# Kernel optimization log

Hardware: AMD Instinct MI355X
Metric: run time of the kernel (lower is better)

Reference implementation:

```python
import jax, jax.numpy as jnp
import numpy as np

N_NODES = 100000
N_EDGES = 1600000
N_GRAPHS = 2048
HID = 64
IN_F = 14
N_CLS = 2
EPS = 1e-5


def _gcn_conv(x, row, col, w_edge, W, b, n_nodes):
    # PyG GCNConv with add_self_loops=True, normalize=True.
    xw = x @ W  # [N, out]
    # degree on target nodes, self-loop contributes weight 1
    deg = jnp.zeros((n_nodes,), x.dtype).at[col].add(w_edge) + 1.0
    dinv = deg ** -0.5
    norm = dinv[row] * w_edge * dinv[col]  # [E]
    out = jnp.zeros_like(xw).at[col].add(norm[:, None] * xw[row])
    out = out + (dinv * dinv)[:, None] * xw  # self-loop term
    return out + b


def _bn_relu(x, gamma, beta):
    mean = jnp.mean(x, axis=0)
    var = jnp.var(x, axis=0)  # biased, as PyTorch BN training normalization
    y = gamma * (x - mean) * jax.lax.rsqrt(var + EPS) + beta
    return jax.nn.relu(y)


def setup_inputs() -> dict:
    key = jax.random.key(0)
    ks = jax.random.split(key, 8)
    x = jax.random.normal(ks[0], (N_NODES, IN_F), dtype=jnp.float32)
    edge_index = jax.random.randint(ks[1], (2, N_EDGES), 0, N_NODES, dtype=jnp.int64)
    batch = jnp.sort(jax.random.randint(ks[2], (N_NODES,), 0, N_GRAPHS, dtype=jnp.int64))
    edge_weight = jnp.ones((N_EDGES,), dtype=jnp.float32)
    def lin(k, fi, fo):
        s = 1.0 / np.sqrt(fi)
        kw, kb = jax.random.split(k)
        return (jax.random.uniform(kw, (fi, fo), jnp.float32, -s, s),
                jax.random.uniform(kb, (fo,), jnp.float32, -s, s))
    W1, b1 = lin(ks[3], IN_F, HID)
    W2, b2 = lin(ks[4], HID, HID)
    W3, b3 = lin(ks[5], HID, HID)
    fcW, fcb = lin(ks[6], HID, N_CLS)
    g = jnp.ones((HID,), jnp.float32)
    z = jnp.zeros((HID,), jnp.float32)
    return {
        "x": x, "edge_index": edge_index, "batch": batch, "edge_weight": edge_weight,
        "W1": W1, "b1": b1, "W2": W2, "b2": b2, "W3": W3, "b3": b3,
        "g1": g, "bt1": z, "g2": g, "bt2": z, "g3": g, "bt3": z,
        "fcW": fcW, "fcb": fcb,
    }


def reference(x, edge_index, batch, edge_weight, W1, b1, W2, b2, W3, b3,
              g1, bt1, g2, bt2, g3, bt3, fcW, fcb):
    row, col = edge_index[0], edge_index[1]
    n = x.shape[0]
    h = _bn_relu(_gcn_conv(x, row, col, edge_weight, W1, b1, n), g1, bt1)
    h = _bn_relu(_gcn_conv(h, row, col, edge_weight, W2, b2, n), g2, bt2)
    h = _bn_relu(_gcn_conv(h, row, col, edge_weight, W3, b3, n), g3, bt3)
    node_embs = h  # dropout p=0 is identity
    graph_emb = jax.ops.segment_sum(node_embs, batch, num_segments=N_GRAPHS)
    out = graph_emb @ fcW + fcb
    return (out, node_embs, graph_emb)
```

## Files before the change

kernel.cpp:

```cpp
#include <hip/hip_runtime.h>

#define N_NODES 100000
#define N_EDGES 1600000
#define EMAX    2400000
#define N_GRAPHS 2048
#define HID 64
#define IN_F 14
#define N_CLS 2
#define EPS 1e-5f

#define BSHIFT 9
#define NBUCK 196
#define ABLOCKS 256
#define CHUNK (N_EDGES / ABLOCKS)

#define NBLK2 128
#define NCHUNK2 ((N_NODES + NBLK2 - 1) / NBLK2)

typedef _Float16 half_t;
typedef _Float16 half8 __attribute__((ext_vector_type(8)));
typedef float f32x4 __attribute__((ext_vector_type(4)));
typedef unsigned int uint4v __attribute__((ext_vector_type(4)));

#define GSTRIDE ((size_t)N_NODES * 16)


__global__ __launch_bounds__(256) void histA_kernel(const int* __restrict__ col,
                                                    int* __restrict__ histG) {
    __shared__ int hl[NBUCK];
    for (int i = threadIdx.x; i < NBUCK; i += 256) hl[i] = 0;
    __syncthreads();
    int e0 = blockIdx.x * CHUNK;
    for (int e = e0 + threadIdx.x; e < e0 + CHUNK; e += 256)
        atomicAdd(&hl[col[e] >> BSHIFT], 1);
    __syncthreads();
    for (int i = threadIdx.x; i < NBUCK; i += 256)
        histG[i * ABLOCKS + blockIdx.x] = hl[i];
}

__global__ __launch_bounds__(256) void scanS1_kernel(const int* __restrict__ histG,
                                                     int* __restrict__ bsumA) {
    __shared__ int ls[256];
    ls[threadIdx.x] = histG[blockIdx.x * 256 + threadIdx.x];
    __syncthreads();
    for (int off = 128; off > 0; off >>= 1) {
        if (threadIdx.x < off) ls[threadIdx.x] += ls[threadIdx.x + off];
        __syncthreads();
    }
    if (threadIdx.x == 0) bsumA[blockIdx.x] = ls[0];
}

__global__ __launch_bounds__(512) void topscan_kernel(int* __restrict__ bsum, int nb) {
    __shared__ int ls[512];
    int t = threadIdx.x;
    int v = (t < nb) ? bsum[t] : 0;
    ls[t] = v;
    __syncthreads();
    for (int off = 1; off < 512; off <<= 1) {
        int x = ls[t];
        if (t >= off) x += ls[t - off];
        __syncthreads();
        ls[t] = x;
        __syncthreads();
    }
    if (t < nb) bsum[t] = ls[t] - v;
}

__global__ __launch_bounds__(256) void scanS3_kernel(int* __restrict__ histG,
                                                     const int* __restrict__ bsumA,
                                                     int* __restrict__ ptr) {
    __shared__ int ls[256];
    int idx = blockIdx.x * 256 + threadIdx.x;
    int v = histG[idx];
    ls[threadIdx.x] = v;
    __syncthreads();
    for (int off = 1; off < 256; off <<= 1) {
        int x = ls[threadIdx.x];
        if (threadIdx.x >= off) x += ls[threadIdx.x - off];
        __syncthreads();
        ls[threadIdx.x] = x;
        __syncthreads();
    }
    histG[idx] = ls[threadIdx.x] - v + bsumA[blockIdx.x];
    if (blockIdx.x == 0 && threadIdx.x == 0) ptr[N_NODES] = N_EDGES;
}

__global__ __launch_bounds__(256) void scatterA_kernel(const int* __restrict__ row,
                                                       const int* __restrict__ col,
                                                       const float* __restrict__ w,
                                                       const int* __restrict__ histG,
                                                       int2* __restrict__ EA) {
    __shared__ int cur[NBUCK];
    for (int i = threadIdx.x; i < NBUCK; i += 256)
        cur[i] = histG[i * ABLOCKS + blockIdx.x];
    __syncthreads();
    int e0 = blockIdx.x * CHUNK;
    for (int e = e0 + threadIdx.x; e < e0 + CHUNK; e += 256) {
        int c = col[e];
        int r = row[e];
        int fx = (int)__float2uint_rn(w[e] * 8192.0f);
        int pos = atomicAdd(&cur[c >> BSHIFT], 1);
        EA[pos] = make_int2(r, (fx << 17) | c);
    }
}

__global__ __launch_bounds__(256) void bucket_kernel(const int2* __restrict__ EA,
                                                     const int* __restrict__ bsumA,
                                                     int2* __restrict__ EB,
                                                     int* __restrict__ ptr,
                                                     float* __restrict__ dinv) {
    __shared__ int hist[512], wsum[512], cur[512];
    int b = blockIdx.x;
    int beg = bsumA[b];
    int end = (b == NBUCK - 1) ? N_EDGES : bsumA[b + 1];
    int i0 = threadIdx.x, i1 = threadIdx.x + 256;
    hist[i0] = 0; hist[i1] = 0;
    wsum[i0] = 0; wsum[i1] = 0;
    __syncthreads();
    for (int e = beg + threadIdx.x; e < end; e += 256) {
        int2 ed = EA[e];
        int c9 = ed.y & 511;
        atomicAdd(&hist[c9], 1);
        atomicAdd(&wsum[c9], (int)((unsigned int)ed.y >> 17));
    }
    __syncthreads();
    int cnt0 = hist[i0], cnt1 = hist[i1];
    for (int off = 1; off < 512; off <<= 1) {
        int v0 = hist[i0], v1 = hist[i1];
        int a0 = (i0 >= off) ? hist[i0 - off] : 0;
        int a1 = (i1 >= off) ? hist[i1 - off] : 0;
        __syncthreads();
        hist[i0] = v0 + a0;
        hist[i1] = v1 + a1;
        __syncthreads();
    }
    int excl0 = hist[i0] - cnt0, excl1 = hist[i1] - cnt1;
    cur[i0] = beg + excl0;
    cur[i1] = beg + excl1;
    int col0 = (b << BSHIFT) + i0, col1 = (b << BSHIFT) + i1;
    if (col0 < N_NODES) {
        ptr[col0] = beg + excl0;
        dinv[col0] = rsqrtf(1.0f + (float)wsum[i0] * (1.0f / 8192.0f));
    }
    if (col1 < N_NODES) {
        ptr[col1] = beg + excl1;
        dinv[col1] = rsqrtf(1.0f + (float)wsum[i1] * (1.0f / 8192.0f));
    }
    __syncthreads();
    for (int e = beg + threadIdx.x; e < end; e += 256) {
        int2 ed = EA[e];
        int pos = atomicAdd(&cur[ed.y & 511], 1);
        EB[pos] = ed;
    }
}


__global__ __launch_bounds__(256) void histD_kernel(const int* __restrict__ ptr,
                                                    int* __restrict__ histD) {
    __shared__ int hl[2048];
    for (int i = threadIdx.x; i < 2048; i += 256) hl[i] = 0;
    __syncthreads();
    int n0 = blockIdx.x * NCHUNK2;
    int n1 = n0 + NCHUNK2; if (n1 > N_NODES) n1 = N_NODES;
    for (int n = n0 + threadIdx.x; n < n1; n += 256) {
        int d = ptr[n + 1] - ptr[n];
        if (d > 255) d = 255;
        atomicAdd(&hl[((threadIdx.x & 7) << 8) + d], 1);
    }
    __syncthreads();
    int s = 0;
#pragma unroll
    for (int c = 0; c < 8; c++) s += hl[(c << 8) + threadIdx.x];
    histD[threadIdx.x * NBLK2 + blockIdx.x] = s;
}

__global__ __launch_bounds__(128) void scanD1_kernel(const int* __restrict__ histD,
                                                     int* __restrict__ rowTot) {
    __shared__ int ls[128];
    ls[threadIdx.x] = histD[blockIdx.x * NBLK2 + threadIdx.x];
    __syncthreads();
    for (int off = 64; off > 0; off >>= 1) {
        if (threadIdx.x < off) ls[threadIdx.x] += ls[threadIdx.x + off];
        __syncthreads();
    }
    if (threadIdx.x == 0) rowTot[blockIdx.x] = ls[0];
}

__global__ __launch_bounds__(256) void topscanD_kernel(const int* __restrict__ rowTot,
                                                       int* __restrict__ nodeExcl,
                                                       int* __restrict__ edgeExcl,
                                                       int* __restrict__ ptrS) {
    __shared__ int a[256], b[256];
    int t = threadIdx.x;
    int cnt = rowTot[t];
    int dpad = (t + 7) & ~7;
    int ec = cnt * dpad;
    a[t] = cnt; b[t] = ec;
    __syncthreads();
    for (int off = 1; off < 256; off <<= 1) {
        int va = a[t], vb = b[t];
        if (t >= off) { va += a[t - off]; vb += b[t - off]; }
        __syncthreads();
        a[t] = va; b[t] = vb;
        __syncthreads();
    }
    nodeExcl[t] = a[t] - cnt;
    edgeExcl[t] = b[t] - ec;
    if (t == 255) ptrS[N_NODES] = b[255];
}

__global__ __launch_bounds__(128) void scanD3_kernel(int* __restrict__ histD,
                                                     const int* __restrict__ nodeExcl) {
    __shared__ int ls[128];
    int idx = blockIdx.x * NBLK2 + threadIdx.x;
    int v = histD[idx];
    ls[threadIdx.x] = v;
    __syncthreads();
    for (int off = 1; off < 128; off <<= 1) {
        int x = ls[threadIdx.x];
        if (threadIdx.x >= off) x += ls[threadIdx.x - off];
        __syncthreads();
        ls[threadIdx.x] = x;
        __syncthreads();
    }
    histD[idx] = ls[threadIdx.x] - v + nodeExcl[blockIdx.x];
}

__global__ __launch_bounds__(256) void scatterD_kernel(const int* __restrict__ ptr,
                                                       const int* __restrict__ histD,
                                                       const int* __restrict__ nodeExcl,
                                                       const int* __restrict__ edgeExcl,
                                                       int* __restrict__ perm,
                                                       int* __restrict__ ptrS,
                                                       int* __restrict__ newbase) {
    __shared__ int cur[256];
    cur[threadIdx.x] = histD[threadIdx.x * NBLK2 + blockIdx.x];
    __syncthreads();
    int n0 = blockIdx.x * NCHUNK2;
    int n1 = n0 + NCHUNK2; if (n1 > N_NODES) n1 = N_NODES;
    for (int n = n0 + threadIdx.x; n < n1; n += 256) {
        int d = ptr[n + 1] - ptr[n];
        if (d > 255) d = 255;
        int dpad = (d + 7) & ~7;
        int pos = atomicAdd(&cur[d], 1);
        int ebase = edgeExcl[d] + (pos - nodeExcl[d]) * dpad;
        perm[pos] = n;
        ptrS[pos] = ebase;
        newbase[n] = ebase;
    }
}

__global__ __launch_bounds__(256) void finalize_kernel(const int2* __restrict__ EB,
                                                       const float* __restrict__ dinv,
                                                       const int* __restrict__ ptr,
                                                       const int* __restrict__ newbase,
                                                       unsigned int* __restrict__ edges, int E) {
    int stride = gridDim.x * blockDim.x;
    for (int e = blockIdx.x * blockDim.x + threadIdx.x; e < E; e += stride) {
        int2 ed = EB[e];
        int c = ed.y & 0x1ffff;
        float w = (float)((unsigned int)ed.y >> 17) * (1.0f / 8192.0f);
        float nrm = dinv[ed.x] * w * dinv[c];
        unsigned int nb = __float_as_uint(nrm);
        unsigned int n15 = (nb + 0x8000u) >> 16;
        if (n15 > 0x7fffu) n15 = 0x7fffu;
        int newpos = newbase[c] + (e - ptr[c]);
        edges[newpos] = ((unsigned int)ed.x << 15) | n15;
    }
}


template <int K>
__global__ __launch_bounds__(256) void gemm_kernel(const float* __restrict__ h,
                                                   const float* __restrict__ W,
                                                   half_t* __restrict__ xw, int n_nodes) {
    int f = threadIdx.x & 63;
    float wcol[K];
#pragma unroll
    for (int k = 0; k < K; k++) wcol[k] = W[k * HID + f];
    half_t* xg = xw + (size_t)(f >> 4) * GSTRIDE + (f & 15);
    int wave = (blockIdx.x * blockDim.x + threadIdx.x) >> 6;
    int nwaves = (gridDim.x * blockDim.x) >> 6;
    for (int n = wave; n < n_nodes; n += nwaves) {
        const float* hr = h + (size_t)n * K;
        float acc = 0.f;
#pragma unroll
        for (int k = 0; k < K; k++) acc += hr[k] * wcol[k];
        xg[(size_t)n * 16] = (half_t)acc;
    }
}

__global__ __launch_bounds__(256) void gemm_bn_mfma_kernel(const half_t* __restrict__ h,
                                                           const float* __restrict__ W,
                                                           const float* __restrict__ stats,
                                                           const float* __restrict__ gamma,
                                                           const float* __restrict__ beta,
                                                           half_t* __restrict__ xw, int n_nodes) {
    __shared__ float sc_s[HID], sh_s[HID];
    if (threadIdx.x < 64) {
        float mean = stats[threadIdx.x] * (1.0f / N_NODES);
        float var = stats[64 + threadIdx.x] * (1.0f / N_NODES) - mean * mean;
        float sc = gamma[threadIdx.x] * rsqrtf(var + EPS);
        sc_s[threadIdx.x] = sc;
        sh_s[threadIdx.x] = beta[threadIdx.x] - mean * sc;
    }
    __syncthreads();
    int lane = threadIdx.x & 63;
    int col16 = lane & 15;
    int quad = lane >> 4;

    float scA[2][8], shA[2][8];
#pragma unroll
    for (int kh = 0; kh < 2; kh++)
#pragma unroll
        for (int j = 0; j < 8; j++) {
            int k = kh * 32 + quad * 8 + j;
            scA[kh][j] = sc_s[k];
            shA[kh][j] = sh_s[k];
        }

    half8 bfrag[4][2];
#pragma unroll
    for (int t = 0; t < 4; t++)
#pragma unroll
        for (int kh = 0; kh < 2; kh++)
#pragma unroll
            for (int j = 0; j < 8; j++) {
                int k = kh * 32 + quad * 8 + j;
                bfrag[t][kh][j] = (half_t)W[k * HID + t * 16 + col16];
            }

    int wave = (blockIdx.x * blockDim.x + threadIdx.x) >> 6;
    int nwaves = (gridDim.x * blockDim.x) >> 6;
    int ntiles = n_nodes >> 4;
    for (int tIdx = wave; tIdx < ntiles; tIdx += nwaves) {
        int n0 = tIdx << 4;
        half8 afrag[2];
#pragma unroll
        for (int kh = 0; kh < 2; kh++) {
            int k0 = kh * 32 + quad * 8;
            const half_t* hp = h + (size_t)(k0 >> 4) * GSTRIDE
                                 + (size_t)(n0 + col16) * 16 + (k0 & 15);
            half8 raw = *(const half8*)hp;
#pragma unroll
            for (int j = 0; j < 8; j++) {
                float v = (float)raw[j] * scA[kh][j] + shA[kh][j];
                afrag[kh][j] = (half_t)fmaxf(v, 0.f);
            }
        }
        f32x4 acc[4];
#pragma unroll
        for (int t = 0; t < 4; t++) {
            f32x4 z = {0.f, 0.f, 0.f, 0.f};
            acc[t] = __builtin_amdgcn_mfma_f32_16x16x32_f16(afrag[0], bfrag[t][0], z, 0, 0, 0);
            acc[t] = __builtin_amdgcn_mfma_f32_16x16x32_f16(afrag[1], bfrag[t][1], acc[t], 0, 0, 0);
        }
#pragma unroll
        for (int t = 0; t < 4; t++) {
            half_t* xg = xw + (size_t)t * GSTRIDE;
#pragma unroll
            for (int r = 0; r < 4; r++) {
                int rowi = n0 + quad * 4 + r;
                xg[(size_t)rowi * 16 + col16] = (half_t)acc[t][r];
            }
        }
    }
}

template <bool LAST>
__global__ __launch_bounds__(256) void gather_stats_kernel(const int* __restrict__ ptrS,
                                                           const int* __restrict__ perm,
                                                           const unsigned int* __restrict__ edges,
                                                           const half_t* __restrict__ xw,
                                                           const float* __restrict__ dinv,
                                                           const float* __restrict__ b,
                                                           half_t* __restrict__ hp,
                                                           float* __restrict__ hf,
                                                           float* __restrict__ stats,
                                                           int n_nodes) {
    int g = (blockIdx.x & 7) >> 1;
    int grank = ((blockIdx.x >> 3) << 1) | (blockIdx.x & 1);
    int lane16 = threadIdx.x & 15;
    int quadLocal = threadIdx.x >> 4;
    int quadId = grank * 16 + quadLocal;
    int nquads = (gridDim.x >> 2) * 16;

    const half_t* xg = xw + (size_t)g * GSTRIDE;
    const char* xgb = (const char*)xg + lane16 * 2;
    half_t* hpg = hp + (size_t)g * GSTRIDE;
    int f = g * 16 + lane16;
    float bf = b[f];

    float s = 0.f, s2 = 0.f;
    for (int i = quadId; i < n_nodes; i += nquads) {
        int node = perm[i];
        int beg = ptrS[i];
        int endp = ptrS[i + 1];
        float a0 = 0.f, a1 = 0.f, a2 = 0.f, a3 = 0.f;
        float a4 = 0.f, a5 = 0.f, a6 = 0.f, a7 = 0.f;
        for (int j = beg; j < endp; j += 8) {
            uint4v p0 = *(const uint4v*)(edges + j);
            uint4v p1 = *(const uint4v*)(edges + j + 4);
            float x0 = (float)*(const half_t*)(xgb + ((size_t)(p0.x >> 15) << 5));
            float x1 = (float)*(const half_t*)(xgb + ((size_t)(p0.y >> 15) << 5));
            float x2 = (float)*(const half_t*)(xgb + ((size_t)(p0.z >> 15) << 5));
            float x3 = (float)*(const half_t*)(xgb + ((size_t)(p0.w >> 15) << 5));
            float x4 = (float)*(const half_t*)(xgb + ((size_t)(p1.x >> 15) << 5));
            float x5 = (float)*(const half_t*)(xgb + ((size_t)(p1.y >> 15) << 5));
            float x6 = (float)*(const half_t*)(xgb + ((size_t)(p1.z >> 15) << 5));
            float x7 = (float)*(const half_t*)(xgb + ((size_t)(p1.w >> 15) << 5));
            a0 += __uint_as_float((p0.x & 0x7fffu) << 16) * x0;
            a1 += __uint_as_float((p0.y & 0x7fffu) << 16) * x1;
            a2 += __uint_as_float((p0.z & 0x7fffu) << 16) * x2;
            a3 += __uint_as_float((p0.w & 0x7fffu) << 16) * x3;
            a4 += __uint_as_float((p1.x & 0x7fffu) << 16) * x4;
            a5 += __uint_as_float((p1.y & 0x7fffu) << 16) * x5;
            a6 += __uint_as_float((p1.z & 0x7fffu) << 16) * x6;
            a7 += __uint_as_float((p1.w & 0x7fffu) << 16) * x7;
        }
        float di = dinv[node];
        float v = (((a0 + a1) + (a2 + a3)) + ((a4 + a5) + (a6 + a7)))
                  + di * di * (float)xg[(size_t)node * 16 + lane16] + bf;
        if (LAST)
            hf[(size_t)node * HID + f] = v;
        else
            hpg[(size_t)node * 16 + lane16] = (half_t)v;
        s += v;
        s2 += v * v;
    }
    __shared__ float ls[256], ls2[256];
    ls[threadIdx.x] = s;
    ls2[threadIdx.x] = s2;
    __syncthreads();
    if (threadIdx.x < 16) {
        float a = 0.f, aa = 0.f;
#pragma unroll
        for (int k = 0; k < 16; k++) {
            a += ls[k * 16 + threadIdx.x];
            aa += ls2[k * 16 + threadIdx.x];
        }
        atomicAdd(&stats[g * 16 + threadIdx.x], a);
        atomicAdd(&stats[64 + g * 16 + threadIdx.x], aa);
    }
}

__global__ __launch_bounds__(256) void bn_relu_seg_kernel(float* __restrict__ h,
                                                          const float* __restrict__ stats,
                                                          const float* __restrict__ gamma,
                                                          const float* __restrict__ beta,
                                                          const int* __restrict__ batch,
                                                          float* __restrict__ gemb,
                                                          int n_nodes) {
    int g = blockIdx.x * blockDim.x + threadIdx.x;
    int f = g & 63;
    int wave = g >> 6;
    int nwaves = (gridDim.x * blockDim.x) >> 6;
    int chunk = (n_nodes + nwaves - 1) / nwaves;
    int n0 = wave * chunk;
    int n1 = n0 + chunk;
    if (n1 > n_nodes) n1 = n_nodes;
    if (n0 >= n_nodes) return;
    float mean = stats[f] * (1.0f / N_NODES);
    float var = stats[64 + f] * (1.0f / N_NODES) - mean * mean;
    float sc = gamma[f] * rsqrtf(var + EPS);
    float sh = beta[f] - mean * sc;
    int curg = batch[n0];
    float racc = 0.f;
    for (int n = n0; n < n1; n++) {
        int bg = batch[n];
        if (bg != curg) {
            atomicAdd(&gemb[(size_t)curg * HID + f], racc);
            racc = 0.f;
            curg = bg;
        }
        size_t idx = (size_t)n * HID + f;
        float v = h[idx] * sc + sh;
        v = fmaxf(v, 0.f);
        h[idx] = v;
        racc += v;
    }
    atomicAdd(&gemb[(size_t)curg * HID + f], racc);
}

__global__ __launch_bounds__(256) void final_kernel(const float* __restrict__ gemb,
                                                    const float* __restrict__ fcW,
                                                    const float* __restrict__ fcb,
                                                    float* __restrict__ out) {
    int g = blockIdx.x * blockDim.x + threadIdx.x;
    if (g >= N_GRAPHS * N_CLS) return;
    int gr = g >> 1, c = g & 1;
    float acc = fcb[c];
#pragma unroll
    for (int k = 0; k < HID; k++) acc += gemb[gr * HID + k] * fcW[k * N_CLS + c];
    out[g] = acc;
}


extern "C" void kernel_launch(void* const* d_in, const int* in_sizes, int n_in,
                              void* d_out, int out_size, void* d_ws, size_t ws_size,
                              hipStream_t stream) {
    const float* x    = (const float*)d_in[0];
    const int*   ei   = (const int*)d_in[1];
    const int*   batch= (const int*)d_in[2];
    const float* ew   = (const float*)d_in[3];
    const float* W1   = (const float*)d_in[4];
    const float* b1   = (const float*)d_in[5];
    const float* W2   = (const float*)d_in[6];
    const float* b2   = (const float*)d_in[7];
    const float* W3   = (const float*)d_in[8];
    const float* b3   = (const float*)d_in[9];
    const float* g1   = (const float*)d_in[10];
    const float* bt1  = (const float*)d_in[11];
    const float* g2   = (const float*)d_in[12];
    const float* bt2  = (const float*)d_in[13];
    const float* g3   = (const float*)d_in[14];
    const float* bt3  = (const float*)d_in[15];
    const float* fcW  = (const float*)d_in[16];
    const float* fcb  = (const float*)d_in[17];

    const int* row = ei;
    const int* col = ei + N_EDGES;

    float* out_head  = (float*)d_out;
    float* node_embs = out_head + N_GRAPHS * N_CLS;
    float* gemb      = node_embs + (size_t)N_NODES * HID;

    char* bse = (char*)d_ws;
    half_t* xwh = (half_t*)bse;
    int2*   EB  = (int2*)bse;
    char* r1 = bse + (size_t)N_NODES * HID * 2;
    int2*   EA  = (int2*)r1;
    half_t* hpl = (half_t*)r1;
    char* r2 = r1 + (size_t)N_NODES * HID * 2;
    unsigned int* edges = (unsigned int*)r2;
    char* r3 = r2 + (size_t)EMAX * 4;
    float* dinv  = (float*)r3;
    float* stats = dinv + N_NODES;
    int*   ptr   = (int*)(stats + 128);
    int*   histG = ptr + N_NODES + 1;
    int*   bsumA = histG + NBUCK * ABLOCKS;
    int*   histD = bsumA + NBUCK + 4;
    int*   rowTot = histD + 256 * NBLK2;
    int*   nodeExcl = rowTot + 256;
    int*   edgeExcl = nodeExcl + 256;
    int*   perm   = edgeExcl + 256;
    int*   newbase= perm + N_NODES;
    int*   ptrS   = newbase + N_NODES;

    const int B   = 256;
    const int gGS = 1024;
    const int gGA = 2048;

    histA_kernel<<<ABLOCKS, B, 0, stream>>>(col, histG);
    scanS1_kernel<<<NBUCK, B, 0, stream>>>(histG, bsumA);
    topscan_kernel<<<1, 512, 0, stream>>>(bsumA, NBUCK);
    scanS3_kernel<<<NBUCK, B, 0, stream>>>(histG, bsumA, ptr);
    scatterA_kernel<<<ABLOCKS, B, 0, stream>>>(row, col, ew, histG, EA);
    bucket_kernel<<<NBUCK, B, 0, stream>>>(EA, bsumA, EB, ptr, dinv);

    histD_kernel<<<NBLK2, B, 0, stream>>>(ptr, histD);
    scanD1_kernel<<<256, 128, 0, stream>>>(histD, rowTot);
    topscanD_kernel<<<1, 256, 0, stream>>>(rowTot, nodeExcl, edgeExcl, ptrS);
    scanD3_kernel<<<256, 128, 0, stream>>>(histD, nodeExcl);
    scatterD_kernel<<<NBLK2, B, 0, stream>>>(ptr, histD, nodeExcl, edgeExcl,
                                             perm, ptrS, newbase);
    hipMemsetAsync(edges, 0, (size_t)EMAX * 4, stream);
    finalize_kernel<<<gGS, B, 0, stream>>>(EB, dinv, ptr, newbase, edges, N_EDGES);

    float* h3 = node_embs;

    gemm_kernel<IN_F><<<gGS, B, 0, stream>>>(x, W1, xwh, N_NODES);
    hipMemsetAsync(stats, 0, 128 * sizeof(float), stream);
    gather_stats_kernel<false><<<gGA, B, 0, stream>>>(ptrS, perm, edges, xwh, dinv,
                                                      b1, hpl, h3, stats, N_NODES);

    gemm_bn_mfma_kernel<<<gGS, B, 0, stream>>>(hpl, W2, stats, g1, bt1, xwh, N_NODES);
    hipMemsetAsync(stats, 0, 128 * sizeof(float), stream);
    gather_stats_kernel<false><<<gGA, B, 0, stream>>>(ptrS, perm, edges, xwh, dinv,
                                                      b2, hpl, h3, stats, N_NODES);

    gemm_bn_mfma_kernel<<<gGS, B, 0, stream>>>(hpl, W3, stats, g2, bt2, xwh, N_NODES);
    hipMemsetAsync(stats, 0, 128 * sizeof(float), stream);
    gather_stats_kernel<true><<<gGA, B, 0, stream>>>(ptrS, perm, edges, xwh, dinv,
                                                     b3, hpl, h3, stats, N_NODES);

    hipMemsetAsync(gemb, 0, (size_t)N_GRAPHS * HID * sizeof(float), stream);
    bn_relu_seg_kernel<<<gGS, B, 0, stream>>>(h3, stats, g3, bt3, batch, gemb, N_NODES);

    final_kernel<<<(N_GRAPHS * N_CLS + B - 1) / B, B, 0, stream>>>(gemb, fcW, fcb, out_head);
}
```

Before: 427.8 us.

## Split edge list into offset and fp16 norm arrays, reduce padding, fuse finalize

Edge storage moves from packed 32-bit words (index plus 15-bit norm) to separate pre-shifted source-offset and fp16 norm arrays. Per-node padding drops from multiples of 8 to multiples of 2, which shrinks the padded edge array. The bucket pass is split so the second half scatters straight into the degree-sorted layout, removing the EB intermediate and the finalize kernel. The gather now loads edges cooperatively across 16 lanes, broadcasts them with shuffles and accumulates in packed half2 FMA. This adds shuffle overhead and loses accumulation precision by summing in fp16.

```diff
diff --git a/kernel.cpp b/kernel.cpp
--- a/kernel.cpp
+++ b/kernel.cpp
@@ -1,8 +1,9 @@
 #include <hip/hip_runtime.h>
+#include <hip/hip_fp16.h>
 
 #define N_NODES 100000
 #define N_EDGES 1600000
-#define EMAX    2400000
+#define EMAX2   1700000
 #define N_GRAPHS 2048
 #define HID 64
 #define IN_F 14
@@ -20,7 +21,6 @@
 typedef _Float16 half_t;
 typedef _Float16 half8 __attribute__((ext_vector_type(8)));
 typedef float f32x4 __attribute__((ext_vector_type(4)));
-typedef unsigned int uint4v __attribute__((ext_vector_type(4)));
 
 #define GSTRIDE ((size_t)N_NODES * 16)
 
@@ -104,12 +104,11 @@
     }
 }
 
-__global__ __launch_bounds__(256) void bucket_kernel(const int2* __restrict__ EA,
-                                                     const int* __restrict__ bsumA,
-                                                     int2* __restrict__ EB,
-                                                     int* __restrict__ ptr,
-                                                     float* __restrict__ dinv) {
-    __shared__ int hist[512], wsum[512], cur[512];
+__global__ __launch_bounds__(256) void bucketA_kernel(const int2* __restrict__ EA,
+                                                      const int* __restrict__ bsumA,
+                                                      int* __restrict__ ptr,
+                                                      float* __restrict__ dinv) {
+    __shared__ int hist[512], wsum[512];
     int b = blockIdx.x;
     int beg = bsumA[b];
     int end = (b == NBUCK - 1) ? N_EDGES : bsumA[b + 1];
@@ -135,8 +134,6 @@
         __syncthreads();
     }
     int excl0 = hist[i0] - cnt0, excl1 = hist[i1] - cnt1;
-    cur[i0] = beg + excl0;
-    cur[i1] = beg + excl1;
     int col0 = (b << BSHIFT) + i0, col1 = (b << BSHIFT) + i1;
     if (col0 < N_NODES) {
         ptr[col0] = beg + excl0;
@@ -145,12 +142,6 @@
     if (col1 < N_NODES) {
         ptr[col1] = beg + excl1;
         dinv[col1] = rsqrtf(1.0f + (float)wsum[i1] * (1.0f / 8192.0f));
-    }
-    __syncthreads();
-    for (int e = beg + threadIdx.x; e < end; e += 256) {
-        int2 ed = EA[e];
-        int pos = atomicAdd(&cur[ed.y & 511], 1);
-        EB[pos] = ed;
     }
 }
 
@@ -193,7 +184,7 @@
     __shared__ int a[256], b[256];
     int t = threadIdx.x;
     int cnt = rowTot[t];
-    int dpad = (t + 7) & ~7;
+    int dpad = (t + 1) & ~1;
     int ec = cnt * dpad;
     a[t] = cnt; b[t] = ec;
     __syncthreads();
@@ -241,7 +232,7 @@
     for (int n = n0 + threadIdx.x; n < n1; n += 256) {
         int d = ptr[n + 1] - ptr[n];
         if (d > 255) d = 255;
-        int dpad = (d + 7) & ~7;
+        int dpad = (d + 1) & ~1;
         int pos = atomicAdd(&cur[d], 1);
         int ebase = edgeExcl[d] + (pos - nodeExcl[d]) * dpad;
         perm[pos] = n;
@@ -250,22 +241,29 @@
     }
 }
 
-__global__ __launch_bounds__(256) void finalize_kernel(const int2* __restrict__ EB,
-                                                       const float* __restrict__ dinv,
-                                                       const int* __restrict__ ptr,
-                                                       const int* __restrict__ newbase,
-                                                       unsigned int* __restrict__ edges, int E) {
-    int stride = gridDim.x * blockDim.x;
-    for (int e = blockIdx.x * blockDim.x + threadIdx.x; e < E; e += stride) {
-        int2 ed = EB[e];
+__global__ __launch_bounds__(256) void bucketB_kernel(const int2* __restrict__ EA,
+                                                      const int* __restrict__ bsumA,
+                                                      const int* __restrict__ newbase,
+                                                      const float* __restrict__ dinv,
+                                                      unsigned int* __restrict__ srcoff,
+                                                      half_t* __restrict__ normh) {
+    __shared__ int cur[512];
+    int b = blockIdx.x;
+    int beg = bsumA[b];
+    int end = (b == NBUCK - 1) ? N_EDGES : bsumA[b + 1];
+    int i0 = threadIdx.x, i1 = threadIdx.x + 256;
+    int col0 = (b << BSHIFT) + i0, col1 = (b << BSHIFT) + i1;
+    cur[i0] = (col0 < N_NODES) ? newbase[col0] : 0;
+    cur[i1] = (col1 < N_NODES) ? newbase[col1] : 0;
+    __syncthreads();
+    for (int e = beg + threadIdx.x; e < end; e += 256) {
+        int2 ed = EA[e];
         int c = ed.y & 0x1ffff;
         float w = (float)((unsigned int)ed.y >> 17) * (1.0f / 8192.0f);
         float nrm = dinv[ed.x] * w * dinv[c];
-        unsigned int nb = __float_as_uint(nrm);
-        unsigned int n15 = (nb + 0x8000u) >> 16;
-        if (n15 > 0x7fffu) n15 = 0x7fffu;
-        int newpos = newbase[c] + (e - ptr[c]);
-        edges[newpos] = ((unsigned int)ed.x << 15) | n15;
+        int pos = atomicAdd(&cur[c & 511], 1);
+        srcoff[pos] = (unsigned int)ed.x << 5;
+        normh[pos] = (half_t)nrm;
     }
 }
 
@@ -370,7 +368,8 @@
 template <bool LAST>
 __global__ __launch_bounds__(256) void gather_stats_kernel(const int* __restrict__ ptrS,
                                                            const int* __restrict__ perm,
-                                                           const unsigned int* __restrict__ edges,
+                                                           const unsigned int* __restrict__ srcoff,
+                                                           const unsigned int* __restrict__ normu,
                                                            const half_t* __restrict__ xw,
                                                            const float* __restrict__ dinv,
                                                            const float* __restrict__ b,
@@ -386,41 +385,58 @@
     int nquads = (gridDim.x >> 2) * 16;
 
     const half_t* xg = xw + (size_t)g * GSTRIDE;
-    const char* xgb = (const char*)xg + lane16 * 2;
+    const char* xgc = (const char*)xg;
+    unsigned int loff = (unsigned int)(lane16 * 2);
     half_t* hpg = hp + (size_t)g * GSTRIDE;
     int f = g * 16 + lane16;
     float bf = b[f];
+    int base = ((threadIdx.x & 63) >> 4) * 16;
 
     float s = 0.f, s2 = 0.f;
     for (int i = quadId; i < n_nodes; i += nquads) {
         int node = perm[i];
         int beg = ptrS[i];
-        int endp = ptrS[i + 1];
-        float a0 = 0.f, a1 = 0.f, a2 = 0.f, a3 = 0.f;
-        float a4 = 0.f, a5 = 0.f, a6 = 0.f, a7 = 0.f;
-        for (int j = beg; j < endp; j += 8) {
-            uint4v p0 = *(const uint4v*)(edges + j);
-            uint4v p1 = *(const uint4v*)(edges + j + 4);
-            float x0 = (float)*(const half_t*)(xgb + ((size_t)(p0.x >> 15) << 5));
-            float x1 = (float)*(const half_t*)(xgb + ((size_t)(p0.y >> 15) << 5));
-            float x2 = (float)*(const half_t*)(xgb + ((size_t)(p0.z >> 15) << 5));
-            float x3 = (float)*(const half_t*)(xgb + ((size_t)(p0.w >> 15) << 5));
-            float x4 = (float)*(const half_t*)(xgb + ((size_t)(p1.x >> 15) << 5));
-            float x5 = (float)*(const half_t*)(xgb + ((size_t)(p1.y >> 15) << 5));
-            float x6 = (float)*(const half_t*)(xgb + ((size_t)(p1.z >> 15) << 5));
-            float x7 = (float)*(const half_t*)(xgb + ((size_t)(p1.w >> 15) << 5));
-            a0 += __uint_as_float((p0.x & 0x7fffu) << 16) * x0;
-            a1 += __uint_as_float((p0.y & 0x7fffu) << 16) * x1;
-            a2 += __uint_as_float((p0.z & 0x7fffu) << 16) * x2;
-            a3 += __uint_as_float((p0.w & 0x7fffu) << 16) * x3;
-            a4 += __uint_as_float((p1.x & 0x7fffu) << 16) * x4;
-            a5 += __uint_as_float((p1.y & 0x7fffu) << 16) * x5;
-            a6 += __uint_as_float((p1.z & 0x7fffu) << 16) * x6;
-            a7 += __uint_as_float((p1.w & 0x7fffu) << 16) * x7;
+        int c = ptrS[i + 1] - beg;
+        __half2 acc0 = __float2half2_rn(0.f);
+        __half2 acc1 = __float2half2_rn(0.f);
+        for (int j0 = 0; j0 < c; j0 += 16) {
+            int m = c - j0;
+            if (m > 16) m = 16;
+            int pairs = m >> 1;
+            int ev = 0, nv = 0;
+            if (lane16 < m) ev = (int)srcoff[beg + j0 + lane16];
+            if (lane16 < pairs) nv = (int)normu[((beg + j0) >> 1) + lane16];
+            int p = 0;
+            for (; p + 2 <= pairs; p += 2) {
+                unsigned int u0 = (unsigned int)__shfl(ev, base + 2 * p);
+                unsigned int u1 = (unsigned int)__shfl(ev, base + 2 * p + 1);
+                unsigned int u2 = (unsigned int)__shfl(ev, base + 2 * p + 2);
+                unsigned int u3 = (unsigned int)__shfl(ev, base + 2 * p + 3);
+                unsigned int nd0 = (unsigned int)__shfl(nv, base + p);
+                unsigned int nd1 = (unsigned int)__shfl(nv, base + p + 1);
+                __half h0 = *(const __half*)(xgc + (u0 + loff));
+                __half h1 = *(const __half*)(xgc + (u1 + loff));
+                __half h2 = *(const __half*)(xgc + (u2 + loff));
+                __half h3 = *(const __half*)(xgc + (u3 + loff));
+                __half2 n01 = *(__half2*)&nd0;
+                __half2 n23 = *(__half2*)&nd1;
+                acc0 = __hfma2(n01, __halves2half2(h0, h1), acc0);
+                acc1 = __hfma2(n23, __halves2half2(h2, h3), acc1);
+            }
+            if (p < pairs) {
+                unsigned int u0 = (unsigned int)__shfl(ev, base + 2 * p);
+                unsigned int u1 = (unsigned int)__shfl(ev, base + 2 * p + 1);
+                unsigned int nd0 = (unsigned int)__shfl(nv, base + p);
+                __half h0 = *(const __half*)(xgc + (u0 + loff));
+                __half h1 = *(const __half*)(xgc + (u1 + loff));
+                __half2 n01 = *(__half2*)&nd0;
+                acc0 = __hfma2(n01, __halves2half2(h0, h1), acc0);
+            }
         }
+        float accf = (__low2float(acc0) + __high2float(acc0))
+                   + (__low2float(acc1) + __high2float(acc1));
         float di = dinv[node];
-        float v = (((a0 + a1) + (a2 + a3)) + ((a4 + a5) + (a6 + a7)))
-                  + di * di * (float)xg[(size_t)node * 16 + lane16] + bf;
+        float v = accf + di * di * (float)xg[(size_t)node * 16 + lane16] + bf;
         if (LAST)
             hf[(size_t)node * HID + f] = v;
         else
@@ -527,13 +543,13 @@
 
     char* bse = (char*)d_ws;
     half_t* xwh = (half_t*)bse;
-    int2*   EB  = (int2*)bse;
     char* r1 = bse + (size_t)N_NODES * HID * 2;
     int2*   EA  = (int2*)r1;
     half_t* hpl = (half_t*)r1;
     char* r2 = r1 + (size_t)N_NODES * HID * 2;
-    unsigned int* edges = (unsigned int*)r2;
-    char* r3 = r2 + (size_t)EMAX * 4;
+    unsigned int* srcoff = (unsigned int*)r2;
+    half_t* normh = (half_t*)(srcoff + EMAX2);
+    char* r3 = r2 + (size_t)EMAX2 * 6;
     float* dinv  = (float*)r3;
     float* stats = dinv + N_NODES;
     int*   ptr   = (int*)(stats + 128);
@@ -556,7 +572,7 @@
     topscan_kernel<<<1, 512, 0, stream>>>(bsumA, NBUCK);
     scanS3_kernel<<<NBUCK, B, 0, stream>>>(histG, bsumA, ptr);
     scatterA_kernel<<<ABLOCKS, B, 0, stream>>>(row, col, ew, histG, EA);
-    bucket_kernel<<<NBUCK, B, 0, stream>>>(EA, bsumA, EB, ptr, dinv);
+    bucketA_kernel<<<NBUCK, B, 0, stream>>>(EA, bsumA, ptr, dinv);
 
     histD_kernel<<<NBLK2, B, 0, stream>>>(ptr, histD);
     scanD1_kernel<<<256, 128, 0, stream>>>(histD, rowTot);
@@ -564,25 +580,28 @@
     scanD3_kernel<<<256, 128, 0, stream>>>(histD, nodeExcl);
     scatterD_kernel<<<NBLK2, B, 0, stream>>>(ptr, histD, nodeExcl, edgeExcl,
                                              perm, ptrS, newbase);
-    hipMemsetAsync(edges, 0, (size_t)EMAX * 4, stream);
-    finalize_kernel<<<gGS, B, 0, stream>>>(EB, dinv, ptr, newbase, edges, N_EDGES);
+    hipMemsetAsync(srcoff, 0, (size_t)EMAX2 * 6, stream);
+    bucketB_kernel<<<NBUCK, B, 0, stream>>>(EA, bsumA, newbase, dinv, srcoff, normh);
 
     float* h3 = node_embs;
 
     gemm_kernel<IN_F><<<gGS, B, 0, stream>>>(x, W1, xwh, N_NODES);
     hipMemsetAsync(stats, 0, 128 * sizeof(float), stream);
-    gather_stats_kernel<false><<<gGA, B, 0, stream>>>(ptrS, perm, edges, xwh, dinv,
-                                                      b1, hpl, h3, stats, N_NODES);
+    gather_stats_kernel<false><<<gGA, B, 0, stream>>>(ptrS, perm, srcoff,
+                                                      (const unsigned int*)normh, xwh,
+                                                      dinv, b1, hpl, h3, stats, N_NODES);
 
     gemm_bn_mfma_kernel<<<gGS, B, 0, stream>>>(hpl, W2, stats, g1, bt1, xwh, N_NODES);
     hipMemsetAsync(stats, 0, 128 * sizeof(float), stream);
-    gather_stats_kernel<false><<<gGA, B, 0, stream>>>(ptrS, perm, edges, xwh, dinv,
-                                                      b2, hpl, h3, stats, N_NODES);
+    gather_stats_kernel<false><<<gGA, B, 0, stream>>>(ptrS, perm, srcoff,
+                                                      (const unsigned int*)normh, xwh,
+                                                      dinv, b2, hpl, h3, stats, N_NODES);
 
     gemm_bn_mfma_kernel<<<gGS, B, 0, stream>>>(hpl, W3, stats, g2, bt2, xwh, N_NODES);
     hipMemsetAsync(stats, 0, 128 * sizeof(float), stream);
-    gather_stats_kernel<true><<<gGA, B, 0, stream>>>(ptrS, perm, edges, xwh, dinv,
-                                                     b3, hpl, h3, stats, N_NODES);
+    gather_stats_kernel<true><<<gGA, B, 0, stream>>>(ptrS, perm, srcoff,
+                                                     (const unsigned int*)normh, xwh,
+                                                     dinv, b3, hpl, h3, stats, N_NODES);
 
     hipMemsetAsync(gemb, 0, (size_t)N_GRAPHS * HID * sizeof(float), stream);
     bn_relu_seg_kernel<<<gGS, B, 0, stream>>>(h3, stats, g3, bt3, batch, gemb, N_NODES);
```

Result: faster. 415.0 us (-3.0%).
